# Kernel tuning notes

Hardware: AMD Instinct MI355X
Metric: run time of the kernel (lower is better)

## Reference

```python
import jax, jax.numpy as jnp
import numpy as np

N_HEADS = 16
EPS = 1e-6  # WanSelfAttention passes eps=1e-6 to WanRMSNorm
ROPE_MAX = 1024


def _rmsnorm(v, g):
    # WanRMSNorm: normalize in fp32 over the full `dim`, then scale by weight
    v32 = v.astype(jnp.float32)
    n = v32 * jax.lax.rsqrt(jnp.mean(v32 * v32, axis=-1, keepdims=True) + EPS)
    return n * g


def _rope(x, f, h, w, fc, fs):
    # x: [b, s, n, d] with s == f*h*w. Complex rope: (a+bi) * (cos + i sin)
    b, s, n, d = x.shape
    c = d // 2
    c1 = c - 2 * (c // 3)
    c2 = c // 3

    def build(t):  # t: [ROPE_MAX, c] -> [1, s, 1, c]
        tf, th, tw = t[:, :c1], t[:, c1:c1 + c2], t[:, c1 + c2:]
        pf = jnp.broadcast_to(tf[:f, None, None, :], (f, h, w, c1))
        ph = jnp.broadcast_to(th[None, :h, None, :], (f, h, w, c2))
        pw = jnp.broadcast_to(tw[None, None, :w, :], (f, h, w, c2))
        return jnp.concatenate([pf, ph, pw], axis=-1).reshape(1, f * h * w, 1, c)

    cosv, sinv = build(fc), build(fs)
    xr = x.astype(jnp.float32).reshape(b, s, n, c, 2)
    a, bi = xr[..., 0], xr[..., 1]
    out_r = a * cosv - bi * sinv
    out_i = a * sinv + bi * cosv
    return jnp.stack([out_r, out_i], axis=-1).reshape(b, s, n, d)


def setup_inputs() -> dict:
    key = jax.random.key(0)
    ks = jax.random.split(key, 12)
    b, s, dim = 1, 2048, 2048
    n, d = N_HEADS, 2048 // N_HEADS  # d = 128, c = 64
    f, h, w = 2, 32, 32              # f*h*w == s
    c = d // 2
    c1 = c - 2 * (c // 3)
    c2 = c // 3

    # Realistic rope tables per band (cos/sin of pos * inv_freq)
    pos = np.arange(ROPE_MAX, dtype=np.float64)[:, None]
    ang = []
    for cx in (c1, c2, c2):
        inv = 1.0 / (10000.0 ** (np.arange(cx, dtype=np.float64) / cx))
        ang.append(pos * inv[None, :])
    ang = np.concatenate(ang, axis=1)
    freqs_cos = jnp.asarray(np.cos(ang), dtype=jnp.float32)
    freqs_sin = jnp.asarray(np.sin(ang), dtype=jnp.float32)

    scale = 1.0 / np.sqrt(dim)
    inp = {
        "x": jax.random.normal(ks[0], (b, s, dim), dtype=jnp.float32),
        "freqs_cos": freqs_cos,
        "freqs_sin": freqs_sin,
        "Wq": jax.random.normal(ks[1], (dim, dim), dtype=jnp.float32) * scale,
        "bq": jnp.zeros((dim,), dtype=jnp.float32),
        "Wk": jax.random.normal(ks[2], (dim, dim), dtype=jnp.float32) * scale,
        "bk": jnp.zeros((dim,), dtype=jnp.float32),
        "Wv": jax.random.normal(ks[3], (dim, dim), dtype=jnp.float32) * scale,
        "bv": jnp.zeros((dim,), dtype=jnp.float32),
        "Wo": jax.random.normal(ks[4], (dim, dim), dtype=jnp.float32) * scale,
        "bo": jnp.zeros((dim,), dtype=jnp.float32),
        "gq": jnp.ones((dim,), dtype=jnp.float32),
        "gk": jnp.ones((dim,), dtype=jnp.float32),
        "seq_lens": jnp.array([s], dtype=jnp.int32),
        "f": f,
        "h": h,
        "w": w,
    }
    return inp


def reference(x, freqs_cos, freqs_sin, Wq, bq, Wk, bk, Wv, bv, Wo, bo, gq, gk,
              seq_lens, f, h, w):
    b, s, dim = x.shape
    n = N_HEADS
    d = dim // n

    q = _rmsnorm(x @ Wq.T + bq, gq).reshape(b, s, n, d)
    k = _rmsnorm(x @ Wk.T + bk, gk).reshape(b, s, n, d)
    v = (x @ Wv.T + bv).reshape(b, s, n, d)

    q = _rope(q, f, h, w, freqs_cos, freqs_sin)
    k = _rope(k, f, h, w, freqs_cos, freqs_sin)

    scale = np.float32(1.0 / np.sqrt(d))
    scores = jnp.einsum('bqnd,bknd->bnqk', q, k) * scale  # [b,n,s,s]
    key_mask = jnp.arange(s)[None, :] < seq_lens[:, None]  # [b,s] (k_lens)
    scores = jnp.where(key_mask[:, None, None, :], scores, -jnp.inf)
    probs = jax.nn.softmax(scores, axis=-1)
    out = jnp.einsum('bnqk,bknd->bqnd', probs, v).reshape(b, s, dim)
    return out @ Wo.T + bo
```

## Files before the change

kernel.cpp:

```cpp
#include <hip/hip_runtime.h>
#include <cstdint>
#include <cmath>

typedef unsigned int uint;
typedef unsigned short ushort;
typedef __bf16 bf16_t;
typedef bf16_t bf16x8 __attribute__((ext_vector_type(8)));
typedef float f32x4 __attribute__((ext_vector_type(4)));
typedef float f32x16 __attribute__((ext_vector_type(16)));

#define LOG2E 1.44269504088896340736f

__device__ __forceinline__ ushort f2bf(float f) {
  uint x = __float_as_uint(f);
  x += 0x7fffu + ((x >> 16) & 1u);
  return (ushort)(x >> 16);
}
__device__ __forceinline__ uint pack2(float lo, float hi) {
  return (uint)f2bf(lo) | ((uint)f2bf(hi) << 16);
}
__device__ __forceinline__ uint cvt_pk_bf16(float lo, float hi) {
  uint r;
  asm("v_cvt_pk_bf16_f32 %0, %1, %2" : "=v"(r) : "v"(lo), "v"(hi));
  return r;
}

__device__ __forceinline__ void gload_lds16(const void* gsrc, void* ldsdst) {
  typedef const __attribute__((address_space(1))) unsigned int* gp_t;
  typedef __attribute__((address_space(3))) unsigned int* lp_t;
  __builtin_amdgcn_global_load_lds((gp_t)(uintptr_t)gsrc,
                                   (lp_t)(unsigned int)(uintptr_t)ldsdst,
                                   16, 0, 0);
}

__global__ __launch_bounds__(256) void cvt_x(const float* __restrict__ src,
                                             ushort* __restrict__ dst, int n8) {
  int i = blockIdx.x * blockDim.x + threadIdx.x;
  if (i >= n8) return;
  const float4* s4 = (const float4*)src;
  float4 a = s4[i * 2], b = s4[i * 2 + 1];
  uint4 o;
  o.x = pack2(a.x, a.y); o.y = pack2(a.z, a.w);
  o.z = pack2(b.x, b.y); o.w = pack2(b.z, b.w);
  ((uint4*)dst)[i] = o;
}

__global__ __launch_bounds__(256) void cvt_w4(const float* __restrict__ s0,
                                              const float* __restrict__ s1,
                                              const float* __restrict__ s2,
                                              const float* __restrict__ s3,
                                              ushort* __restrict__ dA,
                                              ushort* __restrict__ dB, int n8) {
  const int y = blockIdx.y;
  const float* src = (y == 0) ? s0 : (y == 1) ? s1 : (y == 2) ? s2 : s3;
  ushort* dst = (y < 3) ? (dA + (size_t)y * n8 * 8) : dB;
  int i = blockIdx.x * blockDim.x + threadIdx.x;
  if (i >= n8) return;
  const float4* s4 = (const float4*)src;
  float4 a = s4[i * 2], b = s4[i * 2 + 1];
  uint4 o;
  o.x = pack2(a.x, a.y); o.y = pack2(a.z, a.w);
  o.z = pack2(b.x, b.y); o.w = pack2(b.z, b.w);
  ((uint4*)dst)[i] = o;
}

__global__ __launch_bounds__(512) void gemm_qkv(const ushort* __restrict__ A,
                                                const ushort* __restrict__ B,
                                                const float* __restrict__ bq,
                                                const float* __restrict__ bk,
                                                const float* __restrict__ bv,
                                                float* __restrict__ qpre,
                                                float* __restrict__ kpre,
                                                ushort* __restrict__ Vt,
                                                int K, int S_) {
  __shared__ __align__(16) unsigned char As[8192];
  __shared__ __align__(16) unsigned char Bs[8192];
  const int t = threadIdx.x, l = t & 63, w = t >> 6;
  const int g = l >> 4, c = l & 15;
  const int wr = w >> 1, wc = w & 1;
  const int tm = blockIdx.y * 128, tn = blockIdx.x * 128;

  const int srow = w * 16 + (l >> 2);
  const int schunk = (l & 3) ^ (srow & 3);
  const ushort* Ag = A + (size_t)(tm + srow) * K + schunk * 8;
  const ushort* Bg = B + (size_t)(tn + srow) * K + schunk * 8;
  void* AsBase = (void*)(As + w * 1024);
  void* BsBase = (void*)(Bs + w * 1024);

  f32x4 acc[2][4] = {};

  for (int kt = 0; kt < K; kt += 32) {
    __syncthreads();
    gload_lds16(Ag + kt, AsBase);
    gload_lds16(Bg + kt, BsBase);
    __syncthreads();
    bf16x8 af[2], bfr[4];
#pragma unroll
    for (int m = 0; m < 2; ++m) {
      int row = wr * 32 + m * 16 + c;
      af[m] = *(const bf16x8*)(As + row * 64 + ((g ^ (row & 3)) << 4));
    }
#pragma unroll
    for (int n = 0; n < 4; ++n) {
      int row = wc * 64 + n * 16 + c;
      bfr[n] = *(const bf16x8*)(Bs + row * 64 + ((g ^ (row & 3)) << 4));
    }
#pragma unroll
    for (int m = 0; m < 2; ++m)
#pragma unroll
      for (int n = 0; n < 4; ++n)
        acc[m][n] = __builtin_amdgcn_mfma_f32_16x16x32_bf16(af[m], bfr[n], acc[m][n], 0, 0, 0);
  }

  const int sel = tn >> 11;
  if (sel < 2) {
    float* outp = sel ? kpre : qpre;
    const float* bias = sel ? bk : bq;
#pragma unroll
    for (int n = 0; n < 4; ++n) {
      int col = (tn & 2047) + wc * 64 + n * 16 + c;
      float bvv = bias[col];
#pragma unroll
      for (int m = 0; m < 2; ++m) {
        int row0 = tm + wr * 32 + m * 16 + g * 4;
#pragma unroll
        for (int i = 0; i < 4; ++i)
          outp[(size_t)(row0 + i) * 2048 + col] = acc[m][n][i] + bvv;
      }
    }
  } else {
#pragma unroll
    for (int n = 0; n < 4; ++n) {
      int colv = (tn - 4096) + wc * 64 + n * 16 + c;
      float bvv = bv[colv];
#pragma unroll
      for (int m = 0; m < 2; ++m) {
        int row0 = tm + wr * 32 + m * 16 + g * 4;
        uint2 o;
        o.x = pack2(acc[m][n][0] + bvv, acc[m][n][1] + bvv);
        o.y = pack2(acc[m][n][2] + bvv, acc[m][n][3] + bvv);
        *(uint2*)(Vt + (size_t)colv * S_ + row0) = o;
      }
    }
  }
}

__global__ __launch_bounds__(512) void gemm_wo(const ushort* __restrict__ A,
                                               const ushort* __restrict__ B,
                                               float* __restrict__ pbuf, int K) {
  __shared__ __align__(16) unsigned char As[8192];
  __shared__ __align__(16) unsigned char Bs[8192];
  const int t = threadIdx.x, l = t & 63, w = t >> 6;
  const int g = l >> 4, c = l & 15;
  const int wr = w >> 1, wc = w & 1;
  const int tm = blockIdx.y * 128, tn = blockIdx.x * 128;
  const int ks = blockIdx.z;
  const int k0 = ks * (K >> 1), k1 = k0 + (K >> 1);

  const int srow = w * 16 + (l >> 2);
  const int schunk = (l & 3) ^ (srow & 3);
  const ushort* Ag = A + (size_t)(tm + srow) * K + schunk * 8;
  const ushort* Bg = B + (size_t)(tn + srow) * K + schunk * 8;
  void* AsBase = (void*)(As + w * 1024);
  void* BsBase = (void*)(Bs + w * 1024);

  f32x4 acc[2][4] = {};

  for (int kt = k0; kt < k1; kt += 32) {
    __syncthreads();
    gload_lds16(Ag + kt, AsBase);
    gload_lds16(Bg + kt, BsBase);
    __syncthreads();
    bf16x8 af[2], bfr[4];
#pragma unroll
    for (int m = 0; m < 2; ++m) {
      int row = wr * 32 + m * 16 + c;
      af[m] = *(const bf16x8*)(As + row * 64 + ((g ^ (row & 3)) << 4));
    }
#pragma unroll
    for (int n = 0; n < 4; ++n) {
      int row = wc * 64 + n * 16 + c;
      bfr[n] = *(const bf16x8*)(Bs + row * 64 + ((g ^ (row & 3)) << 4));
    }
#pragma unroll
    for (int m = 0; m < 2; ++m)
#pragma unroll
      for (int n = 0; n < 4; ++n)
        acc[m][n] = __builtin_amdgcn_mfma_f32_16x16x32_bf16(af[m], bfr[n], acc[m][n], 0, 0, 0);
  }

  float* out = pbuf + (size_t)ks * 2048 * 2048;
#pragma unroll
  for (int n = 0; n < 4; ++n) {
    int col = tn + wc * 64 + n * 16 + c;
#pragma unroll
    for (int m = 0; m < 2; ++m) {
      int row0 = tm + wr * 32 + m * 16 + g * 4;
#pragma unroll
      for (int i = 0; i < 4; ++i)
        out[(size_t)(row0 + i) * 2048 + col] = acc[m][n][i];
    }
  }
}

__global__ __launch_bounds__(256) void reduce_wo(const float* __restrict__ p,
                                                 const float* __restrict__ bo,
                                                 float* __restrict__ out, int n4) {
  int i = blockIdx.x * blockDim.x + threadIdx.x;
  if (i >= n4) return;
  float4 a = ((const float4*)p)[i];
  float4 b = ((const float4*)p)[i + n4];
  float4 bb = *(const float4*)(bo + ((i * 4) & 2047));
  float4 o;
  o.x = a.x + b.x + bb.x; o.y = a.y + b.y + bb.y;
  o.z = a.z + b.z + bb.z; o.w = a.w + b.w + bb.w;
  ((float4*)out)[i] = o;
}

__global__ __launch_bounds__(256) void fuse_rms_rope(const float* __restrict__ qpre,
                                                     const float* __restrict__ kpre,
                                                     const float* __restrict__ gq,
                                                     const float* __restrict__ gk,
                                                     const float* __restrict__ fc,
                                                     const float* __restrict__ fs,
                                                     const int* __restrict__ pH,
                                                     const int* __restrict__ pW,
                                                     ushort* __restrict__ Qb,
                                                     ushort* __restrict__ Kb,
                                                     int dim, float foldq) {
  const int which = blockIdx.y;
  const float* pre = which ? kpre : qpre;
  const float* gw = which ? gk : gq;
  ushort* outp = which ? Kb : Qb;
  const float fold = which ? 1.0f : foldq;

  const int p = blockIdx.x, t = threadIdx.x;
  const float* row = pre + (size_t)p * dim;
  float v[8];
  {
    float4 a = *(const float4*)(row + t * 8);
    float4 b = *(const float4*)(row + t * 8 + 4);
    v[0] = a.x; v[1] = a.y; v[2] = a.z; v[3] = a.w;
    v[4] = b.x; v[5] = b.y; v[6] = b.z; v[7] = b.w;
  }
  float ss = 0.f;
#pragma unroll
  for (int i = 0; i < 8; ++i) ss += v[i] * v[i];
#pragma unroll
  for (int off = 32; off; off >>= 1) ss += __shfl_xor(ss, off);
  __shared__ float wsum[4];
  if ((t & 63) == 0) wsum[t >> 6] = ss;
  __syncthreads();
  float rstd = rsqrtf((wsum[0] + wsum[1] + wsum[2] + wsum[3]) * (1.0f / dim) + 1e-6f);
  float gv[8];
  {
    float4 a = *(const float4*)(gw + t * 8);
    float4 b = *(const float4*)(gw + t * 8 + 4);
    gv[0] = a.x; gv[1] = a.y; gv[2] = a.z; gv[3] = a.w;
    gv[4] = b.x; gv[5] = b.y; gv[6] = b.z; gv[7] = b.w;
  }
#pragma unroll
  for (int i = 0; i < 8; ++i) v[i] = v[i] * rstd * gv[i];

  const int H = pH[0], W = pW[0];
  const int hw = H * W;
  const int fr = p / hw;
  const int rem = p - fr * hw;
  const int hh = rem / W;
  const int ww = rem - hh * W;
  const int hd = dim / 16;
  const int cd = hd >> 1;
  const int c2 = cd / 3, c1 = cd - 2 * c2;
  const int j0 = ((t * 8) % hd) >> 1;

  uint ob[4];
#pragma unroll
  for (int q = 0; q < 4; ++q) {
    int j = j0 + q;
    int ri = (j < c1) ? fr : ((j < c1 + c2) ? hh : ww);
    float cs = fc[ri * cd + j];
    float sn = fs[ri * cd + j];
    float a = v[2 * q], b = v[2 * q + 1];
    ob[q] = pack2((a * cs - b * sn) * fold, (a * sn + b * cs) * fold);
  }
  uint4 o4; o4.x = ob[0]; o4.y = ob[1]; o4.z = ob[2]; o4.w = ob[3];
  *(uint4*)(outp + (size_t)p * dim + t * 8) = o4;
}

__global__ __launch_bounds__(512, 2) void attn32(const ushort* __restrict__ Qb,
                                                 const ushort* __restrict__ Kb,
                                                 const ushort* __restrict__ Vt,
                                                 ushort* __restrict__ Ob,
                                                 const int* __restrict__ seq_lens,
                                                 int S_, int DIMc) {
  __shared__ __align__(16) unsigned char smem[66560];
  float* mlbuf = (float*)(smem + 65536);
  const int t = threadIdx.x, l = t & 63, w = t >> 6;
  const int qsub = w & 3, ksp = w >> 2;
  const int h = l >> 5, ql = l & 31;

  const int orig = blockIdx.y * gridDim.x + blockIdx.x;
  const int nwg = gridDim.x * gridDim.y;
  const int lin = (orig & 7) * (nwg >> 3) + (orig >> 3);
  const int q0 = (lin % gridDim.x) * 128;
  const int head = lin / gridDim.x;
  const int kvlen = seq_lens[0];

  unsigned char* sk_s = smem + ksp * 16384;
  unsigned char* sv_s = smem + 32768 + ksp * 16384;

  bf16x8 qf[8];
  {
    const ushort* qp = Qb + (size_t)(q0 + qsub * 32 + ql) * DIMc + head * 128 + h * 8;
#pragma unroll
    for (int s = 0; s < 8; ++s) qf[s] = *(const bf16x8*)(qp + s * 16);
  }

  f32x16 ofr[4] = {};
  float m_run = -1e30f, l_run = 0.f;

  const int nt = (kvlen + 63) >> 6;
  const int half = (nt + 1) >> 1;
  const int tbase = ksp ? half : 0;
  const int mycnt = ksp ? (nt - half) : half;

  for (int tt = 0; tt < half; ++tt) {
    __syncthreads();
    if (tt < mycnt) {
      const int kv0 = (tbase + tt) * 64;
#pragma unroll
      for (int it = 0; it < 4; ++it) {
        int kr = qsub * 16 + it * 4 + (l >> 4);
        int kc = (l & 15) ^ (kr & 15);
        gload_lds16(Kb + (size_t)(kv0 + kr) * DIMc + head * 128 + kc * 8,
                    sk_s + qsub * 4096 + it * 1024);
        int vr = qsub * 32 + it * 8 + (l >> 3);
        int vc = (l & 7) ^ (vr & 7);
        gload_lds16(Vt + (size_t)(head * 128 + vr) * S_ + kv0 + vc * 8,
                    sv_s + qsub * 4096 + it * 1024);
      }
    }
    __syncthreads();
    if (tt >= mycnt) continue;
    const int kv0 = (tbase + tt) * 64;

    f32x16 sfr[2] = {};
    __builtin_amdgcn_s_setprio(1);
#pragma unroll
    for (int kb = 0; kb < 2; ++kb) {
      const unsigned char* kbp = sk_s + (kb * 32 + ql) * 256;
      const int rx = (kb * 32 + ql) & 15;
#pragma unroll
      for (int s = 0; s < 8; ++s) {
        bf16x8 kf = *(const bf16x8*)(kbp + (((s * 2 + h) ^ rx) << 4));
        sfr[kb] = __builtin_amdgcn_mfma_f32_32x32x16_bf16(kf, qf[s], sfr[kb], 0, 0, 0);
      }
    }
    __builtin_amdgcn_s_setprio(0);

    if (kv0 + 64 > kvlen) {
#pragma unroll
      for (int kb = 0; kb < 2; ++kb)
#pragma unroll
        for (int r = 0; r < 16; ++r) {
          int key = kv0 + kb * 32 + (r & 3) + 8 * (r >> 2) + 4 * h;
          if (key >= kvlen) sfr[kb][r] = -1e30f;
        }
    }

    float mt = -1e30f;
#pragma unroll
    for (int kb = 0; kb < 2; ++kb)
#pragma unroll
      for (int r = 0; r < 16; ++r) mt = fmaxf(mt, sfr[kb][r]);
    mt = fmaxf(mt, __shfl_xor(mt, 32));

    if (!__all(mt <= m_run + 8.0f)) {
      float m_new = fmaxf(m_run, mt);
      float fac = __builtin_amdgcn_exp2f(m_run - m_new);
      l_run *= fac;
#pragma unroll
      for (int df = 0; df < 4; ++df) ofr[df] *= fac;
      m_run = m_new;
    }

    float ls = 0.f;
    uint u[2][4][2];
#pragma unroll
    for (int kb = 0; kb < 2; ++kb)
#pragma unroll
      for (int G = 0; G < 4; ++G) {
        float p0 = __builtin_amdgcn_exp2f(sfr[kb][G * 4 + 0] - m_run);
        float p1 = __builtin_amdgcn_exp2f(sfr[kb][G * 4 + 1] - m_run);
        float p2 = __builtin_amdgcn_exp2f(sfr[kb][G * 4 + 2] - m_run);
        float p3 = __builtin_amdgcn_exp2f(sfr[kb][G * 4 + 3] - m_run);
        ls += (p0 + p1) + (p2 + p3);
        u[kb][G][0] = cvt_pk_bf16(p0, p1);
        u[kb][G][1] = cvt_pk_bf16(p2, p3);
      }
    ls += __shfl_xor(ls, 32);
    l_run += ls;

#pragma unroll
    for (int ks = 0; ks < 4; ++ks) {
      const int kb = ks >> 1, G0 = (ks & 1) * 2;
      uint own0 = h ? u[kb][G0 + 1][0] : u[kb][G0][0];
      uint own1 = h ? u[kb][G0 + 1][1] : u[kb][G0][1];
      uint snd0 = h ? u[kb][G0][0] : u[kb][G0 + 1][0];
      uint snd1 = h ? u[kb][G0][1] : u[kb][G0 + 1][1];
      uint rcv0 = __shfl_xor(snd0, 32);
      uint rcv1 = __shfl_xor(snd1, 32);
      union { uint4 q; bf16x8 b; } uu;
      uu.q.x = h ? rcv0 : own0;
      uu.q.y = h ? rcv1 : own1;
      uu.q.z = h ? own0 : rcv0;
      uu.q.w = h ? own1 : rcv1;
      __builtin_amdgcn_s_setprio(1);
#pragma unroll
      for (int df = 0; df < 4; ++df) {
        const int row = df * 32 + ql;
        bf16x8 vf = *(const bf16x8*)(sv_s + row * 128 + (((ks * 2 + h) ^ (row & 7)) << 4));
        ofr[df] = __builtin_amdgcn_mfma_f32_32x32x16_bf16(vf, uu.b, ofr[df], 0, 0, 0);
      }
      __builtin_amdgcn_s_setprio(0);
    }
  }

  __syncthreads();
  if (ksp == 1) {
    if (h == 0) { mlbuf[qsub * 64 + ql] = m_run; mlbuf[qsub * 64 + 32 + ql] = l_run; }
    float* ob = (float*)(smem + qsub * 16384);
#pragma unroll
    for (int df = 0; df < 4; ++df)
#pragma unroll
      for (int r = 0; r < 16; ++r) {
        int d = df * 32 + (r & 3) + 8 * (r >> 2) + 4 * h;
        ob[d * 32 + ql] = ofr[df][r];
      }
  }
  __syncthreads();
  if (ksp == 0) {
    float m2 = mlbuf[qsub * 64 + ql], l2 = mlbuf[qsub * 64 + 32 + ql];
    float mstar = fmaxf(m_run, m2);
    float f1 = __builtin_amdgcn_exp2f(m_run - mstar);
    float f2 = (l2 > 0.f) ? __builtin_amdgcn_exp2f(m2 - mstar) : 0.f;
    float lstar = l_run * f1 + l2 * f2;
    float inv = 1.0f / lstar;
    float a1 = f1 * inv, a2 = f2 * inv;
    const float* ob = (const float*)(smem + qsub * 16384);
    ushort* orow = Ob + (size_t)(q0 + qsub * 32 + ql) * DIMc + head * 128;
#pragma unroll
    for (int df = 0; df < 4; ++df)
#pragma unroll
      for (int G = 0; G < 4; ++G) {
        int d0 = df * 32 + 8 * G + 4 * h;
        float v0 = ofr[df][G * 4 + 0] * a1 + ob[(d0 + 0) * 32 + ql] * a2;
        float v1 = ofr[df][G * 4 + 1] * a1 + ob[(d0 + 1) * 32 + ql] * a2;
        float v2 = ofr[df][G * 4 + 2] * a1 + ob[(d0 + 2) * 32 + ql] * a2;
        float v3 = ofr[df][G * 4 + 3] * a1 + ob[(d0 + 3) * 32 + ql] * a2;
        uint2 o; o.x = pack2(v0, v1); o.y = pack2(v2, v3);
        *(uint2*)(orow + d0) = o;
      }
  }
}

extern "C" void kernel_launch(void* const* d_in, const int* in_sizes, int n_in,
                              void* d_out, int out_size, void* d_ws, size_t ws_size,
                              hipStream_t stream) {
  const float* x  = (const float*)d_in[0];
  const float* fc = (const float*)d_in[1];
  const float* fs = (const float*)d_in[2];
  const float* Wq = (const float*)d_in[3];
  const float* bq = (const float*)d_in[4];
  const float* Wk = (const float*)d_in[5];
  const float* bk = (const float*)d_in[6];
  const float* Wv = (const float*)d_in[7];
  const float* bv = (const float*)d_in[8];
  const float* Wo = (const float*)d_in[9];
  const float* bo = (const float*)d_in[10];
  const float* gq = (const float*)d_in[11];
  const float* gk = (const float*)d_in[12];
  const int* seq  = (const int*)d_in[13];
  const int* pH   = (const int*)d_in[15];
  const int* pW   = (const int*)d_in[16];

  const int DIMc = in_sizes[4];
  const int S_   = in_sizes[0] / DIMc;

  char* ws = (char*)d_ws;
  const size_t MB = 1024ull * 1024ull;
  ushort* xb    = (ushort*)(ws + 0 * MB);
  ushort* Wqkvb = (ushort*)(ws + 8 * MB);
  ushort* Wob   = (ushort*)(ws + 32 * MB);
  float*  qpre  = (float*)(ws + 40 * MB);
  float*  kpre  = (float*)(ws + 56 * MB);
  ushort* Qb    = (ushort*)(ws + 72 * MB);
  ushort* Kb    = (ushort*)(ws + 80 * MB);
  ushort* Vt    = (ushort*)(ws + 88 * MB);
  ushort* Ob    = (ushort*)(ws + 40 * MB);
  float*  pbuf  = (float*)(ws + 56 * MB);

  const int nx8 = (S_ * DIMc) / 8;
  const int nw8 = (DIMc * DIMc) / 8;
  cvt_x<<<(nx8 + 255) / 256, 256, 0, stream>>>(x, xb, nx8);
  cvt_w4<<<dim3((nw8 + 255) / 256, 4), 256, 0, stream>>>(Wq, Wk, Wv, Wo, Wqkvb, Wob, nw8);

  gemm_qkv<<<dim3(3 * DIMc / 128, S_ / 128), 512, 0, stream>>>(
      xb, Wqkvb, bq, bk, bv, qpre, kpre, Vt, DIMc, S_);

  const float foldq = LOG2E / sqrtf((float)(DIMc / 16));
  fuse_rms_rope<<<dim3(S_, 2), 256, 0, stream>>>(qpre, kpre, gq, gk, fc, fs, pH, pW,
                                                 Qb, Kb, DIMc, foldq);

  attn32<<<dim3(S_ / 128, 16), 512, 0, stream>>>(Qb, Kb, Vt, Ob, seq, S_, DIMc);

  gemm_wo<<<dim3(16, 16, 2), 512, 0, stream>>>(Ob, Wob, pbuf, DIMc);
  reduce_wo<<<(S_ * DIMc / 4 + 255) / 256, 256, 0, stream>>>(pbuf, bo, (float*)d_out,
                                                             S_ * DIMc / 4);
}
```

Baseline: 190.0 us.

## Rewrite QKV GEMM with 256x256 tiles and double-buffered LDS pipeline

```diff
diff --git a/kernel.cpp b/kernel.cpp
--- a/kernel.cpp
+++ b/kernel.cpp
@@ -64,53 +64,96 @@
   ((uint4*)dst)[i] = o;
 }
 
-__global__ __launch_bounds__(512) void gemm_qkv(const ushort* __restrict__ A,
-                                                const ushort* __restrict__ B,
-                                                const float* __restrict__ bq,
-                                                const float* __restrict__ bk,
-                                                const float* __restrict__ bv,
-                                                float* __restrict__ qpre,
-                                                float* __restrict__ kpre,
-                                                ushort* __restrict__ Vt,
-                                                int K, int S_) {
-  __shared__ __align__(16) unsigned char As[8192];
-  __shared__ __align__(16) unsigned char Bs[8192];
-  const int t = threadIdx.x, l = t & 63, w = t >> 6;
+__global__ __launch_bounds__(512, 2) void gemm_qkv256(const ushort* __restrict__ A,
+                                                      const ushort* __restrict__ B,
+                                                      const float* __restrict__ bq,
+                                                      const float* __restrict__ bk,
+                                                      const float* __restrict__ bv,
+                                                      float* __restrict__ qpre,
+                                                      float* __restrict__ kpre,
+                                                      ushort* __restrict__ Vt,
+                                                      int K, int S_) {
+  __shared__ __align__(16) unsigned char lds[131072];
+  const int t = threadIdx.x, l = t & 63;
+  const int w = t >> 6;
   const int g = l >> 4, c = l & 15;
-  const int wr = w >> 1, wc = w & 1;
-  const int tm = blockIdx.y * 128, tn = blockIdx.x * 128;
-
-  const int srow = w * 16 + (l >> 2);
-  const int schunk = (l & 3) ^ (srow & 3);
+  const int wr = w >> 2, wc = w & 3;
+  const int tm = blockIdx.y * 256, tn = blockIdx.x * 256;
+
+  const int srow = t >> 3;
+  const int schunk = (t & 7) ^ (srow & 7);
   const ushort* Ag = A + (size_t)(tm + srow) * K + schunk * 8;
   const ushort* Bg = B + (size_t)(tn + srow) * K + schunk * 8;
-  void* AsBase = (void*)(As + w * 1024);
-  void* BsBase = (void*)(Bs + w * 1024);
-
-  f32x4 acc[2][4] = {};
-
-  for (int kt = 0; kt < K; kt += 32) {
-    __syncthreads();
-    gload_lds16(Ag + kt, AsBase);
-    gload_lds16(Bg + kt, BsBase);
-    __syncthreads();
-    bf16x8 af[2], bfr[4];
-#pragma unroll
-    for (int m = 0; m < 2; ++m) {
-      int row = wr * 32 + m * 16 + c;
-      af[m] = *(const bf16x8*)(As + row * 64 + ((g ^ (row & 3)) << 4));
-    }
-#pragma unroll
-    for (int n = 0; n < 4; ++n) {
-      int row = wc * 64 + n * 16 + c;
-      bfr[n] = *(const bf16x8*)(Bs + row * 64 + ((g ^ (row & 3)) << 4));
-    }
-#pragma unroll
-    for (int m = 0; m < 2; ++m)
-#pragma unroll
-      for (int n = 0; n < 4; ++n)
-        acc[m][n] = __builtin_amdgcn_mfma_f32_16x16x32_bf16(af[m], bfr[n], acc[m][n], 0, 0, 0);
-  }
+  const size_t rK64 = (size_t)64 * K;
+
+#define STAGE_A(nb, kt) do { const ushort* s_ = Ag + (size_t)(kt) * 64;          \
+    gload_lds16(s_,            lds + (nb) * 32768 + t * 16);                     \
+    gload_lds16(s_ + rK64,     lds + (nb) * 32768 + 8192 + t * 16);              \
+    gload_lds16(s_ + 2 * rK64, lds + (nb) * 32768 + 16384 + t * 16);             \
+    gload_lds16(s_ + 3 * rK64, lds + (nb) * 32768 + 24576 + t * 16); } while (0)
+#define STAGE_B(nb, kt) do { const ushort* s_ = Bg + (size_t)(kt) * 64;          \
+    gload_lds16(s_,            lds + 65536 + (nb) * 32768 + t * 16);             \
+    gload_lds16(s_ + rK64,     lds + 65536 + (nb) * 32768 + 8192 + t * 16);      \
+    gload_lds16(s_ + 2 * rK64, lds + 65536 + (nb) * 32768 + 16384 + t * 16);     \
+    gload_lds16(s_ + 3 * rK64, lds + 65536 + (nb) * 32768 + 24576 + t * 16); } while (0)
+
+  f32x4 acc[8][4] = {};
+  bf16x8 af[2][4], bf[2][4];
+
+#define RD_A(QM) do {                                                            \
+    _Pragma("unroll") for (int ks = 0; ks < 2; ++ks)                             \
+    _Pragma("unroll") for (int mm = 0; mm < 4; ++mm) {                           \
+      int rh = (QM) * 64 + mm * 16 + c;                                          \
+      af[ks][mm] = *(const bf16x8*)(Ab + rh * 128 + (((ks * 4 + g) ^ (rh & 7)) << 4)); } \
+  } while (0)
+#define RD_B() do {                                                              \
+    _Pragma("unroll") for (int ks = 0; ks < 2; ++ks)                             \
+    _Pragma("unroll") for (int nn = 0; nn < 4; ++nn) {                           \
+      int rh = (wc & 1) * 64 + nn * 16 + c;                                      \
+      bf[ks][nn] = *(const bf16x8*)(Bb + rh * 128 + (((ks * 4 + g) ^ (rh & 7)) << 4)); } \
+  } while (0)
+#define MM16(QM, QN) do {                                                        \
+    __builtin_amdgcn_s_barrier();                                                \
+    __builtin_amdgcn_s_setprio(1);                                               \
+    _Pragma("unroll") for (int mm = 0; mm < 4; ++mm)                             \
+    _Pragma("unroll") for (int nn = 0; nn < 2; ++nn) {                           \
+      acc[(QM)*4+mm][(QN)*2+nn] = __builtin_amdgcn_mfma_f32_16x16x32_bf16(       \
+          af[0][mm], bf[0][(QN)*2+nn], acc[(QM)*4+mm][(QN)*2+nn], 0, 0, 0);      \
+      acc[(QM)*4+mm][(QN)*2+nn] = __builtin_amdgcn_mfma_f32_16x16x32_bf16(       \
+          af[1][mm], bf[1][(QN)*2+nn], acc[(QM)*4+mm][(QN)*2+nn], 0, 0, 0); }    \
+    __builtin_amdgcn_s_setprio(0);                                               \
+    __builtin_amdgcn_s_barrier();                                                \
+  } while (0)
+
+  const int NT = K >> 6;
+  STAGE_A(0, 0);
+  STAGE_B(0, 0);
+  asm volatile("s_waitcnt vmcnt(0)" ::: "memory");
+  __builtin_amdgcn_s_barrier();
+
+  for (int j = 0; j < NT; ++j) {
+    const int buf = j & 1, nb = buf ^ 1;
+    const unsigned char* Ab = lds + buf * 32768 + wr * 16384;
+    const unsigned char* Bb = lds + 65536 + buf * 32768 + (wc >> 1) * 16384;
+    const int kt1 = j + 1;
+    const bool st = kt1 < NT;
+    RD_A(0); RD_B();
+    if (st) STAGE_A(nb, kt1);
+    MM16(0, 0);
+    if (st) STAGE_B(nb, kt1);
+    MM16(0, 1);
+    RD_A(1);
+    MM16(1, 0);
+    MM16(1, 1);
+    asm volatile("s_waitcnt vmcnt(0)" ::: "memory");
+    __builtin_amdgcn_s_barrier();
+  }
+
+#undef STAGE_A
+#undef STAGE_B
+#undef RD_A
+#undef RD_B
+#undef MM16
 
   const int sel = tn >> 11;
   if (sel < 2) {
@@ -121,8 +164,8 @@
       int col = (tn & 2047) + wc * 64 + n * 16 + c;
       float bvv = bias[col];
 #pragma unroll
-      for (int m = 0; m < 2; ++m) {
-        int row0 = tm + wr * 32 + m * 16 + g * 4;
+      for (int m = 0; m < 8; ++m) {
+        int row0 = tm + wr * 128 + m * 16 + g * 4;
 #pragma unroll
         for (int i = 0; i < 4; ++i)
           outp[(size_t)(row0 + i) * 2048 + col] = acc[m][n][i] + bvv;
@@ -134,8 +177,8 @@
       int colv = (tn - 4096) + wc * 64 + n * 16 + c;
       float bvv = bv[colv];
 #pragma unroll
-      for (int m = 0; m < 2; ++m) {
-        int row0 = tm + wr * 32 + m * 16 + g * 4;
+      for (int m = 0; m < 8; ++m) {
+        int row0 = tm + wr * 128 + m * 16 + g * 4;
         uint2 o;
         o.x = pack2(acc[m][n][0] + bvv, acc[m][n][1] + bvv);
         o.y = pack2(acc[m][n][2] + bvv, acc[m][n][3] + bvv);
@@ -505,7 +548,7 @@
   cvt_x<<<(nx8 + 255) / 256, 256, 0, stream>>>(x, xb, nx8);
   cvt_w4<<<dim3((nw8 + 255) / 256, 4), 256, 0, stream>>>(Wq, Wk, Wv, Wo, Wqkvb, Wob, nw8);
 
-  gemm_qkv<<<dim3(3 * DIMc / 128, S_ / 128), 512, 0, stream>>>(
+  gemm_qkv256<<<dim3(3 * DIMc / 256, S_ / 256), 512, 0, stream>>>(
       xb, Wqkvb, bq, bk, bv, qpre, kpre, Vt, DIMc, S_);
 
   const float foldq = LOG2E / sqrtf((float)(DIMc / 16));
```

New measurement: 192.8 us. About the same (+1.5%).

## Double-buffer LDS tiles in QKV and Wo GEMMs and merge conversion kernels

Applied to the files above, without the earlier changes.

```diff
diff --git a/kernel.cpp b/kernel.cpp
--- a/kernel.cpp
+++ b/kernel.cpp
@@ -33,8 +33,26 @@
                                    16, 0, 0);
 }
 
-__global__ __launch_bounds__(256) void cvt_x(const float* __restrict__ src,
-                                             ushort* __restrict__ dst, int n8) {
+__global__ __launch_bounds__(256) void cvt5(const float* __restrict__ x,
+                                            const float* __restrict__ wq,
+                                            const float* __restrict__ wk,
+                                            const float* __restrict__ wv,
+                                            const float* __restrict__ wo,
+                                            ushort* __restrict__ xb,
+                                            ushort* __restrict__ wqkv,
+                                            ushort* __restrict__ wob,
+                                            int nx8, int nw8) {
+  const int y = blockIdx.y;
+  const float* src;
+  ushort* dst;
+  int n8;
+  if (y == 0)      { src = x;  dst = xb;  n8 = nx8; }
+  else if (y == 4) { src = wo; dst = wob; n8 = nw8; }
+  else {
+    src = (y == 1) ? wq : (y == 2) ? wk : wv;
+    dst = wqkv + (size_t)(y - 1) * nw8 * 8;
+    n8 = nw8;
+  }
   int i = blockIdx.x * blockDim.x + threadIdx.x;
   if (i >= n8) return;
   const float4* s4 = (const float4*)src;
@@ -45,36 +63,17 @@
   ((uint4*)dst)[i] = o;
 }
 
-__global__ __launch_bounds__(256) void cvt_w4(const float* __restrict__ s0,
-                                              const float* __restrict__ s1,
-                                              const float* __restrict__ s2,
-                                              const float* __restrict__ s3,
-                                              ushort* __restrict__ dA,
-                                              ushort* __restrict__ dB, int n8) {
-  const int y = blockIdx.y;
-  const float* src = (y == 0) ? s0 : (y == 1) ? s1 : (y == 2) ? s2 : s3;
-  ushort* dst = (y < 3) ? (dA + (size_t)y * n8 * 8) : dB;
-  int i = blockIdx.x * blockDim.x + threadIdx.x;
-  if (i >= n8) return;
-  const float4* s4 = (const float4*)src;
-  float4 a = s4[i * 2], b = s4[i * 2 + 1];
-  uint4 o;
-  o.x = pack2(a.x, a.y); o.y = pack2(a.z, a.w);
-  o.z = pack2(b.x, b.y); o.w = pack2(b.z, b.w);
-  ((uint4*)dst)[i] = o;
-}
-
-__global__ __launch_bounds__(512) void gemm_qkv(const ushort* __restrict__ A,
-                                                const ushort* __restrict__ B,
-                                                const float* __restrict__ bq,
-                                                const float* __restrict__ bk,
-                                                const float* __restrict__ bv,
-                                                float* __restrict__ qpre,
-                                                float* __restrict__ kpre,
-                                                ushort* __restrict__ Vt,
-                                                int K, int S_) {
-  __shared__ __align__(16) unsigned char As[8192];
-  __shared__ __align__(16) unsigned char Bs[8192];
+__global__ __launch_bounds__(512) void gemm_qkv_db(const ushort* __restrict__ A,
+                                                   const ushort* __restrict__ B,
+                                                   const float* __restrict__ bq,
+                                                   const float* __restrict__ bk,
+                                                   const float* __restrict__ bv,
+                                                   float* __restrict__ qpre,
+                                                   float* __restrict__ kpre,
+                                                   ushort* __restrict__ Vt,
+                                                   int K, int S_) {
+  __shared__ __align__(16) unsigned char As[16384];
+  __shared__ __align__(16) unsigned char Bs[16384];
   const int t = threadIdx.x, l = t & 63, w = t >> 6;
   const int g = l >> 4, c = l & 15;
   const int wr = w >> 1, wc = w & 1;
@@ -84,32 +83,45 @@
   const int schunk = (l & 3) ^ (srow & 3);
   const ushort* Ag = A + (size_t)(tm + srow) * K + schunk * 8;
   const ushort* Bg = B + (size_t)(tn + srow) * K + schunk * 8;
-  void* AsBase = (void*)(As + w * 1024);
-  void* BsBase = (void*)(Bs + w * 1024);
 
   f32x4 acc[2][4] = {};
 
-  for (int kt = 0; kt < K; kt += 32) {
-    __syncthreads();
-    gload_lds16(Ag + kt, AsBase);
-    gload_lds16(Bg + kt, BsBase);
-    __syncthreads();
+  const int NT = K >> 5;
+  gload_lds16(Ag, As + w * 1024);
+  gload_lds16(Bg, Bs + w * 1024);
+
+  for (int j = 0; j < NT; ++j) {
+    const int buf = j & 1, nb = buf ^ 1;
+    if (j + 1 < NT) {
+      const int kt1 = (j + 1) << 5;
+      gload_lds16(Ag + kt1, As + nb * 8192 + w * 1024);
+      gload_lds16(Bg + kt1, Bs + nb * 8192 + w * 1024);
+      asm volatile("s_waitcnt vmcnt(2)" ::: "memory");
+    } else {
+      asm volatile("s_waitcnt vmcnt(0)" ::: "memory");
+    }
+    __builtin_amdgcn_s_barrier();
+
+    const unsigned char* Ab = As + buf * 8192;
+    const unsigned char* Bb = Bs + buf * 8192;
     bf16x8 af[2], bfr[4];
 #pragma unroll
     for (int m = 0; m < 2; ++m) {
       int row = wr * 32 + m * 16 + c;
-      af[m] = *(const bf16x8*)(As + row * 64 + ((g ^ (row & 3)) << 4));
+      af[m] = *(const bf16x8*)(Ab + row * 64 + ((g ^ (row & 3)) << 4));
     }
 #pragma unroll
     for (int n = 0; n < 4; ++n) {
       int row = wc * 64 + n * 16 + c;
-      bfr[n] = *(const bf16x8*)(Bs + row * 64 + ((g ^ (row & 3)) << 4));
+      bfr[n] = *(const bf16x8*)(Bb + row * 64 + ((g ^ (row & 3)) << 4));
     }
 #pragma unroll
     for (int m = 0; m < 2; ++m)
 #pragma unroll
       for (int n = 0; n < 4; ++n)
         acc[m][n] = __builtin_amdgcn_mfma_f32_16x16x32_bf16(af[m], bfr[n], acc[m][n], 0, 0, 0);
+
+    __builtin_amdgcn_s_barrier();
   }
 
   const int sel = tn >> 11;
@@ -145,48 +157,61 @@
   }
 }
 
-__global__ __launch_bounds__(512) void gemm_wo(const ushort* __restrict__ A,
-                                               const ushort* __restrict__ B,
-                                               float* __restrict__ pbuf, int K) {
-  __shared__ __align__(16) unsigned char As[8192];
-  __shared__ __align__(16) unsigned char Bs[8192];
+__global__ __launch_bounds__(512) void gemm_wo_db(const ushort* __restrict__ A,
+                                                  const ushort* __restrict__ B,
+                                                  float* __restrict__ pbuf, int K) {
+  __shared__ __align__(16) unsigned char As[16384];
+  __shared__ __align__(16) unsigned char Bs[16384];
   const int t = threadIdx.x, l = t & 63, w = t >> 6;
   const int g = l >> 4, c = l & 15;
   const int wr = w >> 1, wc = w & 1;
   const int tm = blockIdx.y * 128, tn = blockIdx.x * 128;
   const int ks = blockIdx.z;
-  const int k0 = ks * (K >> 1), k1 = k0 + (K >> 1);
+  const int k0 = ks * (K >> 1);
 
   const int srow = w * 16 + (l >> 2);
   const int schunk = (l & 3) ^ (srow & 3);
-  const ushort* Ag = A + (size_t)(tm + srow) * K + schunk * 8;
-  const ushort* Bg = B + (size_t)(tn + srow) * K + schunk * 8;
-  void* AsBase = (void*)(As + w * 1024);
-  void* BsBase = (void*)(Bs + w * 1024);
+  const ushort* Ag = A + (size_t)(tm + srow) * K + k0 + schunk * 8;
+  const ushort* Bg = B + (size_t)(tn + srow) * K + k0 + schunk * 8;
 
   f32x4 acc[2][4] = {};
 
-  for (int kt = k0; kt < k1; kt += 32) {
-    __syncthreads();
-    gload_lds16(Ag + kt, AsBase);
-    gload_lds16(Bg + kt, BsBase);
-    __syncthreads();
+  const int NT = K >> 6;
+  gload_lds16(Ag, As + w * 1024);
+  gload_lds16(Bg, Bs + w * 1024);
+
+  for (int j = 0; j < NT; ++j) {
+    const int buf = j & 1, nb = buf ^ 1;
+    if (j + 1 < NT) {
+      const int kt1 = (j + 1) << 5;
+      gload_lds16(Ag + kt1, As + nb * 8192 + w * 1024);
+      gload_lds16(Bg + kt1, Bs + nb * 8192 + w * 1024);
+      asm volatile("s_waitcnt vmcnt(2)" ::: "memory");
+    } else {
+      asm volatile("s_waitcnt vmcnt(0)" ::: "memory");
+    }
+    __builtin_amdgcn_s_barrier();
+
+    const unsigned char* Ab = As + buf * 8192;
+    const unsigned char* Bb = Bs + buf * 8192;
     bf16x8 af[2], bfr[4];
 #pragma unroll
     for (int m = 0; m < 2; ++m) {
       int row = wr * 32 + m * 16 + c;
-      af[m] = *(const bf16x8*)(As + row * 64 + ((g ^ (row & 3)) << 4));
+      af[m] = *(const bf16x8*)(Ab + row * 64 + ((g ^ (row & 3)) << 4));
     }
 #pragma unroll
     for (int n = 0; n < 4; ++n) {
       int row = wc * 64 + n * 16 + c;
-      bfr[n] = *(const bf16x8*)(Bs + row * 64 + ((g ^ (row & 3)) << 4));
+      bfr[n] = *(const bf16x8*)(Bb + row * 64 + ((g ^ (row & 3)) << 4));
     }
 #pragma unroll
     for (int m = 0; m < 2; ++m)
 #pragma unroll
       for (int n = 0; n < 4; ++n)
         acc[m][n] = __builtin_amdgcn_mfma_f32_16x16x32_bf16(af[m], bfr[n], acc[m][n], 0, 0, 0);
+
+    __builtin_amdgcn_s_barrier();
   }
 
   float* out = pbuf + (size_t)ks * 2048 * 2048;
@@ -502,10 +527,11 @@
 
   const int nx8 = (S_ * DIMc) / 8;
   const int nw8 = (DIMc * DIMc) / 8;
-  cvt_x<<<(nx8 + 255) / 256, 256, 0, stream>>>(x, xb, nx8);
-  cvt_w4<<<dim3((nw8 + 255) / 256, 4), 256, 0, stream>>>(Wq, Wk, Wv, Wo, Wqkvb, Wob, nw8);
-
-  gemm_qkv<<<dim3(3 * DIMc / 128, S_ / 128), 512, 0, stream>>>(
+  const int nmax = (nx8 > nw8 ? nx8 : nw8);
+  cvt5<<<dim3((nmax + 255) / 256, 5), 256, 0, stream>>>(x, Wq, Wk, Wv, Wo,
+                                                        xb, Wqkvb, Wob, nx8, nw8);
+
+  gemm_qkv_db<<<dim3(3 * DIMc / 128, S_ / 128), 512, 0, stream>>>(
       xb, Wqkvb, bq, bk, bv, qpre, kpre, Vt, DIMc, S_);
 
   const float foldq = LOG2E / sqrtf((float)(DIMc / 16));
@@ -514,7 +540,7 @@
 
   attn32<<<dim3(S_ / 128, 16), 512, 0, stream>>>(Qb, Kb, Vt, Ob, seq, S_, DIMc);
 
-  gemm_wo<<<dim3(16, 16, 2), 512, 0, stream>>>(Ob, Wob, pbuf, DIMc);
+  gemm_wo_db<<<dim3(16, 16, 2), 512, 0, stream>>>(Ob, Wob, pbuf, DIMc);
   reduce_wo<<<(S_ * DIMc / 4 + 255) / 256, 256, 0, stream>>>(pbuf, bo, (float*)d_out,
                                                              S_ * DIMc / 4);
 }
```

Result: no change. 187.4 us (-1.4%).
